# Kernel optimization log

Hardware: AMD Instinct MI355X
Metric: run time of the kernel (lower is better)

Reference implementation:

```python
import jax, jax.numpy as jnp
import numpy as np

B, NAV, H, W = 16, 36, 120, 160
HID, AEMB, NF = 512, 32, 4

def _conv(x, w, b, stride, pad, dil, groups):
    y = jax.lax.conv_general_dilated(x, w, stride, pad, rhs_dilation=dil, feature_group_count=groups)
    return y + b[None, :, None, None]

def _avgpool(x, k, s):
    y = jax.lax.reduce_window(x, 0.0, jax.lax.add, (1, 1) + k, (1, 1) + s, 'VALID')
    return y / float(k[0] * k[1])

def _conv2_block(x, w1, b1, w2, b2):
    # conv2_1: k5 stride (5,7) dilation 10 -> avgpool 3/3 -> conv2_2: k3 stride 2 dilation (1,2) -> avgpool (3,9)/3
    y = _conv(x, w1, b1, (5, 7), ((0, 0), (0, 0)), (10, 10), 1)
    y = _avgpool(y, (3, 3), (3, 3))
    y = _conv(y, w2, b2, (2, 2), ((0, 0), (0, 0)), (1, 2), 1)
    y = _avgpool(y, (3, 9), (3, 3))
    return y[:, 0]  # [B,3,12]

def setup_inputs() -> dict:
    key = jax.random.key(0)
    ks = jax.random.split(key, 24)
    s = 0.02
    d = {}
    d['depth_feat_0'] = jax.random.normal(ks[0], (B, NAV, H, W), jnp.float32)
    d['depth_feat_1'] = jax.random.normal(ks[1], (B, NAV, H, W), jnp.float32)
    d['obj_detection_feat'] = jax.random.normal(ks[2], (B, NAV, H, W), jnp.float32)
    d['num_navigable_feat'] = jax.random.uniform(ks[3], (B, NAV), jnp.float32)
    d['pre_action_feat'] = jax.random.normal(ks[4], (B, AEMB), jnp.float32)
    d['h_0'] = jax.random.normal(ks[5], (B, HID), jnp.float32)
    d['c_0'] = jax.random.normal(ks[6], (B, HID), jnp.float32)
    d['weighted_ctx'] = jax.random.normal(ks[7], (B, HID), jnp.float32)
    d['navigable_index'] = jax.random.randint(ks[8], (B, 8), 0, NAV).astype(jnp.int32)
    # params
    d['conv1_w'] = jax.random.normal(ks[9], (NAV, 2, 5, 5), jnp.float32) * s
    d['conv1_b'] = jnp.zeros((NAV,), jnp.float32)
    d['dyn_filters'] = jax.random.normal(ks[10], (NF, NAV, 2, 5, 5), jnp.float32) * s
    d['dyn_w1'] = jax.random.normal(ks[11], (HID, HID // 4), jnp.float32) * s
    d['dyn_b1'] = jnp.zeros((HID // 4,), jnp.float32)
    d['dyn_w2'] = jax.random.normal(ks[12], (HID // 4, NF), jnp.float32) * s
    d['dyn_b2'] = jnp.zeros((NF,), jnp.float32)
    d['conv2_1_w'] = jax.random.normal(ks[13], (1, 1, 5, 5), jnp.float32) * s
    d['conv2_1_b'] = jnp.zeros((1,), jnp.float32)
    d['conv2_2_w'] = jax.random.normal(ks[14], (1, 1, 3, 3), jnp.float32) * s
    d['conv2_2_b'] = jnp.zeros((1,), jnp.float32)
    in_sz = HID + NAV + NF + AEMB  # 584
    d['lstm_w_ih'] = jax.random.normal(ks[15], (4 * HID, in_sz), jnp.float32) * s
    d['lstm_w_hh'] = jax.random.normal(ks[16], (4 * HID, HID), jnp.float32) * s
    d['lstm_b_ih'] = jnp.zeros((4 * HID,), jnp.float32)
    d['lstm_b_hh'] = jnp.zeros((4 * HID,), jnp.float32)
    return d

def reference(depth_feat_0, depth_feat_1, obj_detection_feat, num_navigable_feat, pre_action_feat, h_0, c_0, weighted_ctx, navigable_index, conv1_w, conv1_b, dyn_filters, dyn_w1, dyn_b1, dyn_w2, dyn_b2, conv2_1_w, conv2_1_b, conv2_2_w, conv2_2_b, lstm_w_ih, lstm_w_hh, lstm_b_ih, lstm_b_hh):
    Bv = depth_feat_0.shape[0]
    # interleave depth channels: [B,72,H,W] (replaces 36-iter python copy loop)
    mid1 = jnp.stack([depth_feat_0, depth_feat_1], axis=2).reshape(Bv, 2 * NAV, H, W)
    total_depth = _conv(mid1, conv1_w, conv1_b, (1, 1), ((2, 2), (2, 2)), (1, 1), NAV)  # [B,36,H,W]
    nav_attn = jax.nn.softmax(num_navigable_feat, axis=1)[:, :, None, None]
    mid2 = jnp.stack([total_depth * nav_attn, obj_detection_feat * nav_attn], axis=2).reshape(Bv, 2 * NAV, H, W)
    # dynamic conv: per-sample filter = attention-weighted mix of NF learned grouped filters
    filt_attn = jax.nn.softmax(jax.nn.relu(weighted_ctx @ dyn_w1 + dyn_b1) @ dyn_w2 + dyn_b2, axis=1)  # [B,4]
    kern = jnp.einsum('bf,fgikl->bgikl', filt_attn, dyn_filters).reshape(Bv * NAV, 2, 5, 5)
    dyn_out = jax.lax.conv_general_dilated(mid2.reshape(1, Bv * 2 * NAV, H, W), kern, (1, 1), ((2, 2), (2, 2)), feature_group_count=Bv * NAV).reshape(Bv, NAV, H, W)
    # panorama canvas assembly: tile i -> row block (2 - i//12), col i%12
    canvas = dyn_out.reshape(Bv, 3, 12, H, W)[:, ::-1].transpose(0, 1, 3, 2, 4).reshape(Bv, 1, 3 * H, 12 * W)
    v1 = _conv2_block(canvas, conv2_1_w, conv2_1_b, conv2_2_w, conv2_2_b)
    rolled = jnp.concatenate([canvas[..., -W:], canvas[..., :-W]], axis=-1)
    v2 = _conv2_block(rolled, conv2_1_w, conv2_1_b, conv2_2_w, conv2_2_b)
    v2 = jnp.concatenate([v2[:, :, 1:], v2[:, :, :1]], axis=-1)
    vf = ((v1 + v2) * 0.5)[:, ::-1].reshape(Bv, NAV)  # flip row dim then flatten
    vf = jax.nn.softmax(vf / 10.0, axis=1)  # self.softmax_temperature hardcoded to 10
    concat = jnp.concatenate([weighted_ctx, vf, filt_attn, pre_action_feat], axis=1)
    gates = concat @ lstm_w_ih.T + lstm_b_ih + h_0 @ lstm_w_hh.T + lstm_b_hh
    i, f, g, o = jnp.split(gates, 4, axis=1)
    c_1 = jax.nn.sigmoid(f) * c_0 + jax.nn.sigmoid(i) * jnp.tanh(g)
    h_1 = jax.nn.sigmoid(o) * jnp.tanh(c_1)
    mask = jnp.zeros((Bv, NAV + 1), jnp.float32).at[:, 0].set(1.0)
    mask = mask.at[jnp.arange(Bv)[:, None], navigable_index + 1].set(1.0)
    return (h_1, c_1, vf, mask)
```

## Files before the change

### kernel.cpp

```cpp
#include <hip/hip_runtime.h>
#include <math.h>

#define B_ 16
#define NAV_ 36
#define H_ 120
#define W_ 160
#define HID_ 512
#define PLANES (B_*NAV_)
#define PLANE_PX (H_*W_)
#define CANVAS_H 360
#define CANVAS_W 1920
#define CANVAS_PX (CANVAS_H*CANVAS_W)

#define OUT_H 12
#define IN_ROWS 20
#define TD_ROWS 16
#define OBJ_ROWS 16
#define ROWB 352
#define INCH (IN_ROWS*ROWB)
#define NSLOT (2*IN_ROWS*44 + OBJ_ROWS*44)
#define SPT 10

#define WS_NAV    0
#define WS_FATT   576
#define WS_KERN   640
#define WS_TD     29440
#define WS_CANVAS (WS_TD + PLANES*PLANE_PX)
#define WS_POOL1  (WS_CANVAS + B_*CANVAS_PX)
#define WS_VF     (WS_POOL1 + B_*2*19*89)

typedef unsigned int u32;
typedef unsigned short u16;
typedef _Float16 h2_t __attribute__((ext_vector_type(2)));
typedef float float4a __attribute__((ext_vector_type(4), aligned(4)));

__device__ __forceinline__ float sigmoidf_(float x) { return 1.f / (1.f + expf(-x)); }

__device__ __forceinline__ u32 pkh(float a, float b) {
    return __builtin_bit_cast(u32, __builtin_amdgcn_cvt_pkrtz(a, b));
}
__device__ __forceinline__ float h2f(u16 h) {
    _Float16 v = __builtin_bit_cast(_Float16, h);
    return (float)v;
}
__device__ __forceinline__ float dot2h(u32 a, u32 b, float c) {
#if __has_builtin(__builtin_amdgcn_fdot2)
    return __builtin_amdgcn_fdot2(__builtin_bit_cast(h2_t, a),
                                  __builtin_bit_cast(h2_t, b), c, false);
#else
    float r;
    asm("v_dot2_f32_f16 %0, %1, %2, %3" : "=v"(r) : "v"(a), "v"(b), "v"(c));
    return r;
#endif
}

__device__ __forceinline__ void conv8(const unsigned char* b0, const unsigned char* b1,
                                      const u32* ew, float* acc)
{
    #pragma unroll
    for (int ky = 0; ky < 5; ++ky) {
        const int off = ky*ROWB;
        int4 qa = *(const int4*)(b0 + off);
        int2 qb = *(const int2*)(b0 + off + 16);
        int4 ra = *(const int4*)(b1 + off);
        int2 rb = *(const int2*)(b1 + off + 16);
        u32 P[6] = {(u32)qa.x,(u32)qa.y,(u32)qa.z,(u32)qa.w,(u32)qb.x,(u32)qb.y};
        u32 Q[6] = {(u32)ra.x,(u32)ra.y,(u32)ra.z,(u32)ra.w,(u32)rb.x,(u32)rb.y};
        const u32 e0 = ew[ky*3+0], e1 = ew[ky*3+1], e2 = ew[ky*3+2];
        const u32 f0 = ew[15+ky*3+0], f1 = ew[15+ky*3+1], f2 = ew[15+ky*3+2];
        const u32 o0 = e0 << 16;
        const u32 o1 = __builtin_amdgcn_alignbit(e1, e0, 16);
        const u32 o2 = __builtin_amdgcn_alignbit(e2, e1, 16);
        const u32 g0 = f0 << 16;
        const u32 g1 = __builtin_amdgcn_alignbit(f1, f0, 16);
        const u32 g2 = __builtin_amdgcn_alignbit(f2, f1, 16);
        #pragma unroll
        for (int m = 0; m < 4; ++m) {
            acc[2*m]   = dot2h(e0, P[m], dot2h(e1, P[m+1], dot2h(e2, P[m+2], acc[2*m])));
            acc[2*m+1] = dot2h(o0, P[m], dot2h(o1, P[m+1], dot2h(o2, P[m+2], acc[2*m+1])));
            acc[2*m]   = dot2h(f0, Q[m], dot2h(f1, Q[m+1], dot2h(f2, Q[m+2], acc[2*m])));
            acc[2*m+1] = dot2h(g0, Q[m], dot2h(g1, Q[m+1], dot2h(g2, Q[m+2], acc[2*m+1])));
        }
    }
}

#define LOAD_EW(EW, SW)                                                        \
    {                                                                          \
        _Pragma("unroll")                                                      \
        for (int q = 0; q < 7; ++q) {                                          \
            int4 t_ = ((const int4*)(SW))[q];                                  \
            EW[4*q]=(u32)t_.x; EW[4*q+1]=(u32)t_.y; EW[4*q+2]=(u32)t_.z; EW[4*q+3]=(u32)t_.w; \
        }                                                                      \
        int2 t_ = ((const int2*)(SW))[14];                                     \
        EW[28]=(u32)t_.x; EW[29]=(u32)t_.y;                                    \
    }

__global__ __launch_bounds__(256)
void k_pre(const float* __restrict__ wctx, const float* __restrict__ dw1,
           const float* __restrict__ db1, const float* __restrict__ dw2,
           const float* __restrict__ db2, const float* __restrict__ dynf,
           const float* __restrict__ numnav, float* __restrict__ ws)
{
    const int tid = threadIdx.x;
    const int b = blockIdx.x;
    __shared__ float sh[128];
    __shared__ float sred[8];
    __shared__ float nv[36];
    __shared__ float nms[2];
    if (tid < 128) {
        float acc = db1[tid];
        for (int k = 0; k < HID_; ++k) acc += wctx[b*HID_ + k] * dw1[k*128 + tid];
        sh[tid] = fmaxf(acc, 0.f);
    }
    __syncthreads();
    if (tid < 4) {
        float acc = db2[tid];
        for (int j = 0; j < 128; ++j) acc += sh[j] * dw2[j*4 + tid];
        sred[tid] = acc;
    }
    __syncthreads();
    if (tid == 0) {
        float m = fmaxf(fmaxf(sred[0], sred[1]), fmaxf(sred[2], sred[3]));
        float e0 = expf(sred[0]-m), e1 = expf(sred[1]-m), e2 = expf(sred[2]-m), e3 = expf(sred[3]-m);
        float s = e0+e1+e2+e3;
        sred[4] = e0/s; sred[5] = e1/s; sred[6] = e2/s; sred[7] = e3/s;
        ws[WS_FATT + b*4+0] = sred[4]; ws[WS_FATT + b*4+1] = sred[5];
        ws[WS_FATT + b*4+2] = sred[6]; ws[WS_FATT + b*4+3] = sred[7];
    }
    __syncthreads();
    {
        const float fa0 = sred[4], fa1 = sred[5], fa2 = sred[6], fa3 = sred[7];
        for (int e = tid; e < 1800; e += 256) {
            float v = fa0*dynf[e] + fa1*dynf[1800+e] + fa2*dynf[3600+e] + fa3*dynf[5400+e];
            ws[WS_KERN + b*1800 + e] = v;
        }
    }
    if (tid < 36) nv[tid] = numnav[b*NAV_ + tid];
    __syncthreads();
    if (tid == 0) {
        float m = nv[0];
        for (int i = 1; i < 36; ++i) m = fmaxf(m, nv[i]);
        float s = 0.f;
        for (int i = 0; i < 36; ++i) s += expf(nv[i]-m);
        nms[0] = m; nms[1] = s;
    }
    __syncthreads();
    if (tid < 36) ws[WS_NAV + b*NAV_ + tid] = expf(nv[tid]-nms[0]) / nms[1];
}

__global__ __launch_bounds__(256)
void k_fused(const float* __restrict__ d0, const float* __restrict__ d1,
             const float* __restrict__ obj, const float* __restrict__ conv1_w,
             const float* __restrict__ conv1_b, float* __restrict__ ws)
{
    const int tid = threadIdx.x;
    const int half = blockIdx.x;
    const int plane = blockIdx.y;
    const int b = plane / NAV_;
    const int g = plane % NAV_;
    const int r0base = half * 5 * OUT_H;

    __shared__ __align__(16) unsigned char smem[2*INCH + OBJ_ROWS*ROWB + TD_ROWS*ROWB + 256];
    unsigned char* inL  = smem;
    unsigned char* objL = smem + 2*INCH;
    unsigned char* tdL  = objL + OBJ_ROWS*ROWB;
    u32* wts = (u32*)(tdL + TD_ROWS*ROWB);

    if (tid < 30) {
        const int ch = tid/15, ky = (tid%15)/3, k = tid%3;
        const float* wsrc = conv1_w + g*50 + ch*25 + ky*5;
        wts[tid] = pkh(wsrc[2*k], (k < 2) ? wsrc[2*k+1] : 0.f);
    } else if (tid >= 32 && tid < 62) {
        const int t2 = tid - 32;
        const int ch = t2/15, ky = (t2%15)/3, k = t2%3;
        const float* wsrc = ws + WS_KERN + plane*50 + ch*25 + ky*5;
        wts[tid] = pkh(wsrc[2*k], (k < 2) ? wsrc[2*k+1] : 0.f);
    } else if (tid == 62) ((float*)wts)[62] = conv1_b[g];
    else if (tid == 63)   ((float*)wts)[63] = ws[WS_NAV + plane];
    if (tid >= 64 && tid < 96) {
        const int t2 = tid - 64;
        const int rr = t2 >> 1;
        *(u32*)(tdL + rr*ROWB + ((t2 & 1) ? 324 : 0)) = 0;
    }

    const float* pd0 = d0 + (size_t)plane*PLANE_PX;
    const float* pd1 = d1 + (size_t)plane*PLANE_PX;
    const float* pob = obj + (size_t)plane*PLANE_PX;

    u32 meta[SPT];
    #pragma unroll
    for (int k = 0; k < SPT; ++k) {
        const int slot = tid + 256*k;
        u32 m = 0;
        if (slot < NSLOT) {
            int j, rr4, ss; u32 dst;
            if (slot < 2*IN_ROWS*44) {
                const int ch = slot / (IN_ROWS*44);
                const int rem = slot % (IN_ROWS*44);
                const int row = rem / 44;
                j = rem % 44; rr4 = row; ss = ch;
                dst = (u32)(ch*INCH + row*ROWB + j*8);
            } else {
                const int s2 = slot - 2*IN_ROWS*44;
                const int row = s2 / 44;
                j = s2 % 44; rr4 = row + 2; ss = 2;
                dst = (u32)(2*INCH + row*ROWB + j*8);
            }
            m = dst | ((u32)j << 15) | ((u32)rr4 << 21) | ((u32)ss << 26) | 0x80000000u;
        }
        meta[k] = m;
    }

    float4a pf[SPT];
    const float4a z4 = {0.f, 0.f, 0.f, 0.f};

    #define ISSUE(R0) {                                                        \
        _Pragma("unroll")                                                      \
        for (int k = 0; k < SPT; ++k) {                                        \
            float4a v = z4;                                                    \
            if (meta[k] & 0x80000000u) {                                       \
                const int j   = (int)((meta[k] >> 15) & 63u);                  \
                const int gr  = (R0) + (int)((meta[k] >> 21) & 31u) - 4;       \
                const int ss  = (int)((meta[k] >> 26) & 3u);                   \
                if ((unsigned)gr < (unsigned)H_ && j <= 40) {                  \
                    const float* src = (ss == 0) ? pd0 : ((ss == 1) ? pd1 : pob); \
                    const int co = (j == 0) ? 0 : ((j < 40) ? 4*j - 2 : 156);  \
                    v = *(const float4a*)(src + gr*W_ + co);                   \
                }                                                              \
            }                                                                  \
            pf[k] = v;                                                         \
        } }

    #define WRITEPF() {                                                        \
        _Pragma("unroll")                                                      \
        for (int k = 0; k < SPT; ++k) {                                        \
            if (meta[k] & 0x80000000u) {                                       \
                const int j = (int)((meta[k] >> 15) & 63u);                    \
                u32 lo = 0, hi = 0;                                            \
                if (j == 0)       { hi = pkh(pf[k].x, pf[k].y); }              \
                else if (j < 40)  { lo = pkh(pf[k].x, pf[k].y); hi = pkh(pf[k].z, pf[k].w); } \
                else if (j == 40) { lo = pkh(pf[k].z, pf[k].w); }              \
                *(int2*)(smem + (meta[k] & 0x7FFFu)) = make_int2((int)lo, (int)hi); \
            }                                                                  \
        } }

    ISSUE(r0base)
    WRITEPF()
    __syncthreads();

    for (int band = 0; band < 5; ++band) {
        const int r0 = r0base + band*OUT_H;
        if (band < 4) ISSUE(r0 + OUT_H)

        for (int t = tid; t < TD_ROWS*20; t += 256) {
            const int tr = t/20, s = t%20;
            const int gr = r0 - 2 + tr;
            u32* rowp = (u32*)(tdL + tr*ROWB);
            if ((unsigned)gr >= (unsigned)H_) {
                rowp[4*s+1] = 0;
                *(int2*)(rowp + 4*s + 2) = make_int2(0, 0);
                rowp[4*s+4] = 0;
                continue;
            }
            float acc[8];
            #pragma unroll
            for (int p = 0; p < 8; ++p) acc[p] = 0.f;
            u32 ew[30];
            LOAD_EW(ew, wts)
            conv8(inL + tr*ROWB + s*16, inL + INCH + tr*ROWB + s*16, ew, acc);
            const float bias = ((const float*)wts)[62];
            const u32 p0 = pkh(acc[0]+bias, acc[1]+bias);
            const u32 p1 = pkh(acc[2]+bias, acc[3]+bias);
            const u32 p2 = pkh(acc[4]+bias, acc[5]+bias);
            const u32 p3 = pkh(acc[6]+bias, acc[7]+bias);
            rowp[4*s+1] = p0;
            *(int2*)(rowp + 4*s + 2) = make_int2((int)p1, (int)p2);
            rowp[4*s+4] = p3;
        }
        __syncthreads();

        if (tid < OUT_H*20) {
            const int yr = tid/20, s = tid%20;
            float acc[8];
            #pragma unroll
            for (int p = 0; p < 8; ++p) acc[p] = 0.f;
            u32 ew[30];
            LOAD_EW(ew, wts + 32)
            conv8(tdL + yr*ROWB + s*16, objL + yr*ROWB + s*16, ew, acc);
            const float a = ((const float*)wts)[63];
            const int rowblk = 2 - g/12;
            const int colblk = g % 12;
            u16* cb = (u16*)(ws + WS_CANVAS) + (size_t)b*CANVAS_PX
                    + (size_t)(rowblk*H_ + r0 + yr)*CANVAS_W + colblk*W_ + s*8;
            const u32 q0 = pkh(a*acc[0], a*acc[1]);
            const u32 q1 = pkh(a*acc[2], a*acc[3]);
            const u32 q2 = pkh(a*acc[4], a*acc[5]);
            const u32 q3 = pkh(a*acc[6], a*acc[7]);
            *(int4*)cb = make_int4((int)q0, (int)q1, (int)q2, (int)q3);
        }
        __syncthreads();

        if (band < 4) {
            WRITEPF()
            __syncthreads();
        }
    }
}

__global__ __launch_bounds__(256)
void k_conv2a(const float* __restrict__ w21p, const float* __restrict__ b21p,
              float* __restrict__ ws)
{
    const int a = blockIdx.x;
    const int b = blockIdx.y;
    const int tid = threadIdx.x;

    __shared__ __align__(16) u16 cvh[11*CANVAS_W];
    __shared__ float s1[2*801];
    __shared__ float swt[25];
    if (tid < 25) swt[tid] = w21p[tid];
    const float b21 = b21p[0];

    const u16* cvsrc = (const u16*)(ws + WS_CANVAS) + (size_t)b*CANVAS_PX;
    for (int i = tid; i < 11*240; i += 256) {
        const int k = i / 240;
        const int c8 = i % 240;
        *(int4*)&cvh[k*CANVAS_W + c8*8] =
            *(const int4*)(cvsrc + (size_t)(15*a + 5*k)*CANVAS_W + c8*8);
    }
    __syncthreads();

    for (int t = tid; t < 2*801; t += 256) {
        const int ver = t / 801;
        const int px = t % 801;
        const int row = px / 267;
        const int v = px % 267;
        const int coloff = ver ? (CANVAS_W - W_) : 0;
        float acc = b21;
        #pragma unroll
        for (int ky = 0; ky < 5; ++ky) {
            const u16* rp = &cvh[(row + 2*ky)*CANVAS_W];
            #pragma unroll
            for (int kx = 0; kx < 5; ++kx) {
                int c = 7*v + 10*kx + coloff;
                if (c >= CANVAS_W) c -= CANVAS_W;
                acc += swt[ky*5+kx] * h2f(rp[c]);
            }
        }
        s1[ver*801 + px] = acc;
    }
    __syncthreads();

    if (tid < 2*89) {
        const int ver = tid / 89;
        const int bb = tid % 89;
        float s = 0.f;
        #pragma unroll
        for (int i = 0; i < 3; ++i)
            #pragma unroll
            for (int j = 0; j < 3; ++j)
                s += s1[ver*801 + i*267 + 3*bb + j];
        ws[WS_POOL1 + ((b*2 + ver)*19 + a)*89 + bb] = s * (1.f/9.f);
    }
}

__global__ __launch_bounds__(256)
void k_conv2b(const float* __restrict__ w22p, const float* __restrict__ b22p,
              const int* __restrict__ navidx, float* __restrict__ ws,
              float* __restrict__ out)
{
    const int b = blockIdx.x;
    __shared__ float p[2*19*89];
    __shared__ float s2[2*9*43];
    __shared__ float svf[36];
    __shared__ float sms[2];
    __shared__ float swt[9];

    for (int i = threadIdx.x; i < 2*19*89; i += 256)
        p[i] = ws[WS_POOL1 + (b*2)*19*89 + i];
    if (threadIdx.x < 9) swt[threadIdx.x] = w22p[threadIdx.x];
    const float b22 = b22p[0];
    __syncthreads();

    for (int t = threadIdx.x; t < 2*9*43; t += 256) {
        const int ver = t / 387;
        const int r = t % 387;
        const int pp = r / 43;
        const int q = r % 43;
        float acc = b22;
        #pragma unroll
        for (int i = 0; i < 3; ++i)
            #pragma unroll
            for (int j = 0; j < 3; ++j)
                acc += swt[i*3+j] * p[(ver*19 + (2*pp+i))*89 + 2*q + 2*j];
        s2[ver*387 + pp*43 + q] = acc;
    }
    __syncthreads();

    if (threadIdx.x < 36) {
        const int gg = threadIdx.x;
        const int io = 2 - gg/12;
        const int j  = gg % 12;
        const int j2 = (j + 1) % 12;
        float s = 0.f;
        #pragma unroll
        for (int ii = 0; ii < 3; ++ii)
            #pragma unroll
            for (int jj = 0; jj < 9; ++jj)
                s += s2[(3*io+ii)*43 + 3*j + jj] + s2[387 + (3*io+ii)*43 + 3*j2 + jj];
        svf[gg] = s * (0.5f/27.f);
    }
    __syncthreads();
    if (threadIdx.x == 0) {
        float m = svf[0];
        for (int i = 1; i < 36; ++i) m = fmaxf(m, svf[i]);
        float s = 0.f;
        for (int i = 0; i < 36; ++i) s += expf((svf[i]-m)*0.1f);
        sms[0] = m; sms[1] = s;
    }
    __syncthreads();
    if (threadIdx.x < 36) {
        const float v = expf((svf[threadIdx.x]-sms[0])*0.1f) / sms[1];
        ws[WS_VF + b*36 + threadIdx.x] = v;
        out[16384 + b*36 + threadIdx.x] = v;
    }
    if (threadIdx.x < 37) {
        const int j = threadIdx.x;
        float v = (j == 0) ? 1.f : 0.f;
        #pragma unroll
        for (int t = 0; t < 8; ++t)
            if (navidx[b*8+t] + 1 == j) v = 1.f;
        out[16960 + b*37 + j] = v;
    }
}

#define CT_STRIDE 17
__global__ __launch_bounds__(256)
void k_lstm(const float* __restrict__ wctx, const float* __restrict__ pre_action,
            const float* __restrict__ h0, const float* __restrict__ c0,
            const float* __restrict__ w_ih, const float* __restrict__ w_hh,
            const float* __restrict__ b_ih, const float* __restrict__ b_hh,
            const float* __restrict__ ws, float* __restrict__ out)
{
    __shared__ float cT[1096*CT_STRIDE];
    __shared__ float red[8*32*16];
    __shared__ float gatev[8][16];
    const int tid = threadIdx.x;

    for (int idx = tid; idx < 1096*16; idx += 256) {
        const int bb = idx / 1096;
        const int k = idx - bb*1096;
        float v;
        if (k < 512)       v = wctx[bb*512 + k];
        else if (k < 548)  v = ws[WS_VF + bb*36 + (k-512)];
        else if (k < 552)  v = ws[WS_FATT + bb*4 + (k-548)];
        else if (k < 584)  v = pre_action[bb*32 + (k-552)];
        else               v = h0[bb*512 + (k-584)];
        cT[k*CT_STRIDE + bb] = v;
    }
    __syncthreads();

    const int rl = tid >> 5;
    const int lane = tid & 31;
    const int u0 = blockIdx.x*2;
    const int ul = rl & 1;
    const int gate = rl >> 1;
    const int r = u0 + ul + gate*512;

    float acc[16];
    #pragma unroll
    for (int i = 0; i < 16; ++i) acc[i] = 0.f;

    const float* wih_r = w_ih + (size_t)r*584;
    for (int k = lane; k < 584; k += 32) {
        const float wv = wih_r[k];
        const float* cp = cT + k*CT_STRIDE;
        #pragma unroll
        for (int i = 0; i < 16; ++i) acc[i] += wv*cp[i];
    }
    const float* whh_r = w_hh + (size_t)r*512;
    for (int k = lane; k < 512; k += 32) {
        const float wv = whh_r[k];
        const float* cp = cT + (584+k)*CT_STRIDE;
        #pragma unroll
        for (int i = 0; i < 16; ++i) acc[i] += wv*cp[i];
    }
    float* rp = red + (rl*32 + lane)*16;
    #pragma unroll
    for (int i = 0; i < 16; ++i) rp[i] = acc[i];
    __syncthreads();

    if (tid < 128) {
        const int rr = tid >> 4;
        const int bb = tid & 15;
        const int rrow = u0 + (rr & 1) + (rr >> 1)*512;
        float s = b_ih[rrow] + b_hh[rrow];
        for (int l = 0; l < 32; ++l) s += red[(rr*32 + l)*16 + bb];
        gatev[rr][bb] = s;
    }
    __syncthreads();

    if (tid < 32) {
        const int ul2 = tid >> 4;
        const int bb = tid & 15;
        const int u = u0 + ul2;
        const float gi = gatev[0+ul2][bb];
        const float gf = gatev[2+ul2][bb];
        const float gg = gatev[4+ul2][bb];
        const float go = gatev[6+ul2][bb];
        const float c1 = sigmoidf_(gf)*c0[bb*512+u] + sigmoidf_(gi)*tanhf(gg);
        const float h1 = sigmoidf_(go)*tanhf(c1);
        out[bb*512 + u] = h1;
        out[8192 + bb*512 + u] = c1;
    }
}

extern "C" void kernel_launch(void* const* d_in, const int* in_sizes, int n_in,
                              void* d_out, int out_size, void* d_ws, size_t ws_size,
                              hipStream_t stream)
{
    const float* d0        = (const float*)d_in[0];
    const float* d1        = (const float*)d_in[1];
    const float* obj       = (const float*)d_in[2];
    const float* numnav    = (const float*)d_in[3];
    const float* preact    = (const float*)d_in[4];
    const float* h0        = (const float*)d_in[5];
    const float* c0        = (const float*)d_in[6];
    const float* wctx      = (const float*)d_in[7];
    const int*   navidx    = (const int*)d_in[8];
    const float* conv1_w   = (const float*)d_in[9];
    const float* conv1_b   = (const float*)d_in[10];
    const float* dynf      = (const float*)d_in[11];
    const float* dw1       = (const float*)d_in[12];
    const float* db1       = (const float*)d_in[13];
    const float* dw2       = (const float*)d_in[14];
    const float* db2       = (const float*)d_in[15];
    const float* w21       = (const float*)d_in[16];
    const float* b21       = (const float*)d_in[17];
    const float* w22       = (const float*)d_in[18];
    const float* b22       = (const float*)d_in[19];
    const float* wih       = (const float*)d_in[20];
    const float* whh       = (const float*)d_in[21];
    const float* bih       = (const float*)d_in[22];
    const float* bhh       = (const float*)d_in[23];
    float* ws  = (float*)d_ws;
    float* out = (float*)d_out;

    dim3 blk(256);
    k_pre   <<<dim3(16),      blk, 0, stream>>>(wctx, dw1, db1, dw2, db2, dynf, numnav, ws);
    k_fused <<<dim3(2, 576),  blk, 0, stream>>>(d0, d1, obj, conv1_w, conv1_b, ws);
    k_conv2a<<<dim3(19, 16),  blk, 0, stream>>>(w21, b21, ws);
    k_conv2b<<<dim3(16),      blk, 0, stream>>>(w22, b22, navidx, ws, out);
    k_lstm  <<<dim3(256),     blk, 0, stream>>>(wctx, preact, h0, c0, wih, whh,
                                                bih, bhh, ws, out);
}
```

Measured before the change: 137.4 us.

## Fold dynamic-filter prelude into fused conv kernel, removing k_pre launch

Removes the separate k_pre kernel. Each k_fused block now recomputes the 512x128 MLP, the filter softmax, the mixed dynamic kernel for its own plane and the navigable softmax, after issuing its first global prefetch so the latency can overlap. This drops one launch and a serial dependency, but every one of the 1152 blocks redundantly runs a 512-iteration dot-product loop on 128 threads. It also adds three extra barriers before the main loop.

```diff
diff --git a/kernel.cpp b/kernel.cpp
--- a/kernel.cpp
+++ b/kernel.cpp
@@ -96,62 +96,13 @@
     }
 
 __global__ __launch_bounds__(256)
-void k_pre(const float* __restrict__ wctx, const float* __restrict__ dw1,
-           const float* __restrict__ db1, const float* __restrict__ dw2,
-           const float* __restrict__ db2, const float* __restrict__ dynf,
-           const float* __restrict__ numnav, float* __restrict__ ws)
-{
-    const int tid = threadIdx.x;
-    const int b = blockIdx.x;
-    __shared__ float sh[128];
-    __shared__ float sred[8];
-    __shared__ float nv[36];
-    __shared__ float nms[2];
-    if (tid < 128) {
-        float acc = db1[tid];
-        for (int k = 0; k < HID_; ++k) acc += wctx[b*HID_ + k] * dw1[k*128 + tid];
-        sh[tid] = fmaxf(acc, 0.f);
-    }
-    __syncthreads();
-    if (tid < 4) {
-        float acc = db2[tid];
-        for (int j = 0; j < 128; ++j) acc += sh[j] * dw2[j*4 + tid];
-        sred[tid] = acc;
-    }
-    __syncthreads();
-    if (tid == 0) {
-        float m = fmaxf(fmaxf(sred[0], sred[1]), fmaxf(sred[2], sred[3]));
-        float e0 = expf(sred[0]-m), e1 = expf(sred[1]-m), e2 = expf(sred[2]-m), e3 = expf(sred[3]-m);
-        float s = e0+e1+e2+e3;
-        sred[4] = e0/s; sred[5] = e1/s; sred[6] = e2/s; sred[7] = e3/s;
-        ws[WS_FATT + b*4+0] = sred[4]; ws[WS_FATT + b*4+1] = sred[5];
-        ws[WS_FATT + b*4+2] = sred[6]; ws[WS_FATT + b*4+3] = sred[7];
-    }
-    __syncthreads();
-    {
-        const float fa0 = sred[4], fa1 = sred[5], fa2 = sred[6], fa3 = sred[7];
-        for (int e = tid; e < 1800; e += 256) {
-            float v = fa0*dynf[e] + fa1*dynf[1800+e] + fa2*dynf[3600+e] + fa3*dynf[5400+e];
-            ws[WS_KERN + b*1800 + e] = v;
-        }
-    }
-    if (tid < 36) nv[tid] = numnav[b*NAV_ + tid];
-    __syncthreads();
-    if (tid == 0) {
-        float m = nv[0];
-        for (int i = 1; i < 36; ++i) m = fmaxf(m, nv[i]);
-        float s = 0.f;
-        for (int i = 0; i < 36; ++i) s += expf(nv[i]-m);
-        nms[0] = m; nms[1] = s;
-    }
-    __syncthreads();
-    if (tid < 36) ws[WS_NAV + b*NAV_ + tid] = expf(nv[tid]-nms[0]) / nms[1];
-}
-
-__global__ __launch_bounds__(256)
 void k_fused(const float* __restrict__ d0, const float* __restrict__ d1,
              const float* __restrict__ obj, const float* __restrict__ conv1_w,
-             const float* __restrict__ conv1_b, float* __restrict__ ws)
+             const float* __restrict__ conv1_b, const float* __restrict__ wctx,
+             const float* __restrict__ dw1, const float* __restrict__ db1,
+             const float* __restrict__ dw2, const float* __restrict__ db2,
+             const float* __restrict__ dynf, const float* __restrict__ numnav,
+             float* __restrict__ ws)
 {
     const int tid = threadIdx.x;
     const int half = blockIdx.x;
@@ -161,27 +112,14 @@
     const int r0base = half * 5 * OUT_H;
 
     __shared__ __align__(16) unsigned char smem[2*INCH + OBJ_ROWS*ROWB + TD_ROWS*ROWB + 256];
+    __shared__ float sh[128];
+    __shared__ float sfa[8];
+    __shared__ float nv[36];
+    __shared__ float snav[1];
     unsigned char* inL  = smem;
     unsigned char* objL = smem + 2*INCH;
     unsigned char* tdL  = objL + OBJ_ROWS*ROWB;
     u32* wts = (u32*)(tdL + TD_ROWS*ROWB);
-
-    if (tid < 30) {
-        const int ch = tid/15, ky = (tid%15)/3, k = tid%3;
-        const float* wsrc = conv1_w + g*50 + ch*25 + ky*5;
-        wts[tid] = pkh(wsrc[2*k], (k < 2) ? wsrc[2*k+1] : 0.f);
-    } else if (tid >= 32 && tid < 62) {
-        const int t2 = tid - 32;
-        const int ch = t2/15, ky = (t2%15)/3, k = t2%3;
-        const float* wsrc = ws + WS_KERN + plane*50 + ch*25 + ky*5;
-        wts[tid] = pkh(wsrc[2*k], (k < 2) ? wsrc[2*k+1] : 0.f);
-    } else if (tid == 62) ((float*)wts)[62] = conv1_b[g];
-    else if (tid == 63)   ((float*)wts)[63] = ws[WS_NAV + plane];
-    if (tid >= 64 && tid < 96) {
-        const int t2 = tid - 64;
-        const int rr = t2 >> 1;
-        *(u32*)(tdL + rr*ROWB + ((t2 & 1) ? 324 : 0)) = 0;
-    }
 
     const float* pd0 = d0 + (size_t)plane*PLANE_PX;
     const float* pd1 = d1 + (size_t)plane*PLANE_PX;
@@ -245,6 +183,67 @@
         } }
 
     ISSUE(r0base)
+
+    if (tid < 128) {
+        float acc = db1[tid];
+        for (int k = 0; k < HID_; ++k) acc += wctx[b*HID_ + k] * dw1[k*128 + tid];
+        sh[tid] = fmaxf(acc, 0.f);
+    } else if (tid < 158) {
+        const int t2 = tid - 128;
+        const int ch = t2/15, ky = (t2%15)/3, k = t2%3;
+        const float* wsrc = conv1_w + g*50 + ch*25 + ky*5;
+        wts[t2] = pkh(wsrc[2*k], (k < 2) ? wsrc[2*k+1] : 0.f);
+    } else if (tid == 158) {
+        ((float*)wts)[62] = conv1_b[g];
+    } else if (tid >= 160 && tid < 192) {
+        const int t2 = tid - 160;
+        const int rr = t2 >> 1;
+        *(u32*)(tdL + rr*ROWB + ((t2 & 1) ? 324 : 0)) = 0;
+    } else if (tid >= 192 && tid < 228) {
+        nv[tid - 192] = numnav[b*NAV_ + (tid - 192)];
+    }
+    __syncthreads();
+
+    if (tid < 4) {
+        float acc = db2[tid];
+        for (int j = 0; j < 128; ++j) acc += sh[j] * dw2[j*4 + tid];
+        sfa[tid] = acc;
+    } else if (tid == 4) {
+        float m = nv[0];
+        for (int i = 1; i < 36; ++i) m = fmaxf(m, nv[i]);
+        float s = 0.f;
+        for (int i = 0; i < 36; ++i) s += expf(nv[i]-m);
+        snav[0] = expf(nv[g]-m) / s;
+    }
+    __syncthreads();
+
+    if (tid == 0) {
+        float m = fmaxf(fmaxf(sfa[0], sfa[1]), fmaxf(sfa[2], sfa[3]));
+        float e0 = expf(sfa[0]-m), e1 = expf(sfa[1]-m), e2 = expf(sfa[2]-m), e3 = expf(sfa[3]-m);
+        float s = e0+e1+e2+e3;
+        sfa[4] = e0/s; sfa[5] = e1/s; sfa[6] = e2/s; sfa[7] = e3/s;
+    }
+    __syncthreads();
+
+    if (tid < 30) {
+        const int ch = tid/15, ky = (tid%15)/3, k = tid%3;
+        const int base = g*50 + ch*25 + ky*5;
+        const float fa0 = sfa[4], fa1 = sfa[5], fa2 = sfa[6], fa3 = sfa[7];
+        const int i0 = 2*k;
+        const float v0 = fa0*dynf[base+i0] + fa1*dynf[1800+base+i0]
+                       + fa2*dynf[3600+base+i0] + fa3*dynf[5400+base+i0];
+        float v1 = 0.f;
+        if (k < 2) {
+            const int i1 = 2*k + 1;
+            v1 = fa0*dynf[base+i1] + fa1*dynf[1800+base+i1]
+               + fa2*dynf[3600+base+i1] + fa3*dynf[5400+base+i1];
+        }
+        wts[32 + tid] = pkh(v0, v1);
+    } else if (tid == 30) {
+        ((float*)wts)[63] = snav[0];
+    } else if (half == 0 && g == 0 && tid >= 32 && tid < 36) {
+        ws[WS_FATT + b*4 + (tid - 32)] = sfa[4 + (tid - 32)];
+    }
     WRITEPF()
     __syncthreads();
 
@@ -547,8 +546,9 @@
     float* out = (float*)d_out;
 
     dim3 blk(256);
-    k_pre   <<<dim3(16),      blk, 0, stream>>>(wctx, dw1, db1, dw2, db2, dynf, numnav, ws);
-    k_fused <<<dim3(2, 576),  blk, 0, stream>>>(d0, d1, obj, conv1_w, conv1_b, ws);
+    k_fused <<<dim3(2, 576),  blk, 0, stream>>>(d0, d1, obj, conv1_w, conv1_b,
+                                                wctx, dw1, db1, dw2, db2, dynf,
+                                                numnav, ws);
     k_conv2a<<<dim3(19, 16),  blk, 0, stream>>>(w21, b21, ws);
     k_conv2b<<<dim3(16),      blk, 0, stream>>>(w22, b22, navidx, ws, out);
     k_lstm  <<<dim3(256),     blk, 0, stream>>>(wctx, preact, h0, c0, wih, whh,
```

Measured after the change: 147.9 us. +7.6%, slower.
